# Kernel tuning notes

Hardware: AMD Instinct MI355X
Metric: run time of the kernel (lower is better)

## Reference

```python
import jax, jax.numpy as jnp
import numpy as np

B, S, HID, NH, AH, F = 1024, 100, 128, 2, 64, 2
DH = HID // NH          # item/pos head size = 64
DA = AH // NH           # attribute head size = 32
EPS = 1e-12


def setup_inputs() -> dict:
    key = jax.random.key(0)
    ks = iter(jax.random.split(key, 32))
    n = lambda shape, s=0.02: jax.random.normal(next(ks), shape, dtype=jnp.float32) * s
    inp = {
        "input_tensor": jax.random.normal(next(ks), (B, S, HID), dtype=jnp.float32),
        "attribute_table": jax.random.normal(next(ks), (F, B, S, AH), dtype=jnp.float32),
        "position_embedding": jax.random.normal(next(ks), (B, S, HID), dtype=jnp.float32),
        "attention_mask": jnp.zeros((B, 1, S, S), dtype=jnp.float32),
        # item / positional projections (stored [in, out])
        "Wq": n((HID, HID)), "bq": jnp.zeros((HID,), jnp.float32),
        "Wk": n((HID, HID)), "bk": jnp.zeros((HID,), jnp.float32),
        "Wv": n((HID, HID)), "bv": jnp.zeros((HID,), jnp.float32),
        "Wqp": n((HID, HID)), "bqp": jnp.zeros((HID,), jnp.float32),
        "Wkp": n((HID, HID)), "bkp": jnp.zeros((HID,), jnp.float32),
        # per-attribute projections, stacked over feat axis
        "Wq_attr": n((F, AH, AH)), "bq_attr": jnp.zeros((F, AH), jnp.float32),
        "Wk_attr": n((F, AH, AH)), "bk_attr": jnp.zeros((F, AH), jnp.float32),
        # gate fusion (VanillaAttentionX): Linear(S,S) -> ReLU -> Linear(S,1)
        "fuse_W1": n((S, S)), "fuse_b1": jnp.zeros((S,), jnp.float32),
        "fuse_W2": n((S, 1)), "fuse_b2": jnp.zeros((1,), jnp.float32),
        # output dense + LayerNorm
        "Wd": n((HID, HID)), "bd": jnp.zeros((HID,), jnp.float32),
        "ln_g": jnp.ones((HID,), jnp.float32), "ln_b": jnp.zeros((HID,), jnp.float32),
    }
    return inp


def _split_heads(x, nh):  # [B,S,nh*d] -> [B,nh,S,d]
    b, s, hd = x.shape
    return x.reshape(b, s, nh, hd // nh).transpose(0, 2, 1, 3)


def reference(input_tensor, attribute_table, position_embedding, attention_mask,
              Wq, bq, Wk, bk, Wv, bv, Wqp, bqp, Wkp, bkp,
              Wq_attr, bq_attr, Wk_attr, bk_attr,
              fuse_W1, fuse_b1, fuse_W2, fuse_b2,
              Wd, bd, ln_g, ln_b):
    b, s, hid = input_tensor.shape
    # item / positional QKV
    q = _split_heads(input_tensor @ Wq + bq, NH)
    k = _split_heads(input_tensor @ Wk + bk, NH)
    v = _split_heads(input_tensor @ Wv + bv, NH)
    qp = _split_heads(position_embedding @ Wqp + bqp, NH)
    kp = _split_heads(position_embedding @ Wkp + bkp, NH)
    item_scores = jnp.einsum('bhqd,bhkd->bhqk', q, k)
    pos_scores = jnp.einsum('bhqd,bhkd->bhqk', qp, kp)
    # attribute score streams: [F,B,S,AH] -> [F,B,NH,S,DA]
    aq = jnp.einsum('fbsa,fao->fbso', attribute_table, Wq_attr) + bq_attr[:, None, None, :]
    ak = jnp.einsum('fbsa,fao->fbso', attribute_table, Wk_attr) + bk_attr[:, None, None, :]
    aq = aq.reshape(F, b, s, NH, DA).transpose(0, 1, 3, 2, 4)
    ak = ak.reshape(F, b, s, NH, DA).transpose(0, 1, 3, 2, 4)
    attr_scores = jnp.einsum('fbhqd,fbhkd->fbhqk', aq, ak)  # [F,B,NH,S,S]
    # gate fusion: stack streams on axis -2 -> [B,NH,S,F+2,S]
    stacked = jnp.concatenate([
        jnp.moveaxis(attr_scores, 0, 3),
        item_scores[:, :, :, None, :],
        pos_scores[:, :, :, None, :],
    ], axis=-2)
    energy = jax.nn.relu(stacked @ fuse_W1 + fuse_b1) @ fuse_W2 + fuse_b2  # [B,NH,S,F+2,1]
    gate_w = jax.nn.softmax(energy[..., 0], axis=-1)                       # [B,NH,S,F+2]
    fused = jnp.einsum('bhsfk,bhsf->bhsk', stacked, gate_w)                # [B,NH,S,S]
    scores = fused / jnp.sqrt(jnp.asarray(DH, fused.dtype)) + attention_mask
    probs = jax.nn.softmax(scores, axis=-1)
    ctx = jnp.einsum('bhqk,bhkd->bhqd', probs, v)
    ctx = ctx.transpose(0, 2, 1, 3).reshape(b, s, hid)
    h = ctx @ Wd + bd + input_tensor
    mu = jnp.mean(h, axis=-1, keepdims=True)
    var = jnp.mean((h - mu) ** 2, axis=-1, keepdims=True)
    return (h - mu) / jnp.sqrt(var + EPS) * ln_g + ln_b
```

## Files before the change

kernel.cpp:

```cpp
#include <hip/hip_runtime.h>
#include <hip/hip_bf16.h>

using bf16 = __hip_bfloat16;
using u16 = unsigned short;
typedef __attribute__((ext_vector_type(8))) short bf16x8;
typedef __attribute__((ext_vector_type(16))) float f32x16;

namespace {

constexpr int B_  = 1024;
constexpr int Sd  = 100;
constexpr int BS_ = B_ * Sd;

constexpr int NTHR = 1024;
constexpr int NW   = 16;

constexpr int STP = 420;
constexpr int STS = 104;
constexpr int QKP = 196;
constexpr int AP  = 132;
constexpr int ATP = 68;
constexpr int W1P = 116;
constexpr int VTP = 116;

constexpr int O_ST = 0;
constexpr int O_Q  = 84000;
constexpr int O_K  = 123200;
constexpr int E2S  = 32000;
constexpr int LBYTES = 162400;

constexpr int WQT_E  = 0;
constexpr int WKT_E  = 16384;
constexpr int WQPT_E = 32768;
constexpr int WKPT_E = 49152;
constexpr int WVT_E  = 65536;
constexpr int WAT_E  = 81920;
constexpr int W1T_E  = 98304;
constexpr int WDT_E  = 113152;
constexpr size_t WS_NEED = 129536ull * 2;

__device__ __forceinline__ float bfr(u16 u) {
  unsigned int x = ((unsigned int)u) << 16;
  float f; __builtin_memcpy(&f, &x, 4); return f;
}
__device__ __forceinline__ u16 f2bu(float x) {
  bf16 h = __float2bfloat16(x);
  u16 u; __builtin_memcpy(&u, &h, 2); return u;
}
__device__ __forceinline__ float4 ld4(const float* p) {
  return *reinterpret_cast<const float4*>(p);
}
__device__ __forceinline__ float wsum(float v) {
#pragma unroll
  for (int m = 32; m > 0; m >>= 1) v += __shfl_xor(v, m);
  return v;
}
__device__ __forceinline__ float wmax(float v) {
#pragma unroll
  for (int m = 32; m > 0; m >>= 1) v = fmaxf(v, __shfl_xor(v, m));
  return v;
}

__device__ __forceinline__ f32x16 zf16() {
  f32x16 z;
#pragma unroll
  for (int i = 0; i < 16; ++i) z[i] = 0.f;
  return z;
}
__device__ __forceinline__ f32x16 MFMA32(bf16x8 a, bf16x8 b, f32x16 c) {
  return __builtin_amdgcn_mfma_f32_32x32x16_bf16(a, b, c, 0, 0, 0);
}

__device__ __forceinline__ bf16x8 ld8(const u16* p) {
  const ushort4 a = *reinterpret_cast<const ushort4*>(p);
  const ushort4 b = *reinterpret_cast<const ushort4*>(p + 4);
  bf16x8 f;
  f[0] = (short)a.x; f[1] = (short)a.y; f[2] = (short)a.z; f[3] = (short)a.w;
  f[4] = (short)b.x; f[5] = (short)b.y; f[6] = (short)b.z; f[7] = (short)b.w;
  return f;
}

template <int L4>
__device__ __forceinline__ void stage_rows4(const float* __restrict__ src, u16* dst,
                                            int nrow, int pitch, int tid, int nthr) {
  for (int i = tid; i < (nrow << L4); i += nthr) {
    const int rr = i >> L4, cc = (i & ((1 << L4) - 1)) << 2;
    const float4 v = *reinterpret_cast<const float4*>(src + ((size_t)rr << (L4 + 2)) + cc);
    ushort4 o;
    o.x = f2bu(v.x); o.y = f2bu(v.y); o.z = f2bu(v.z); o.w = f2bu(v.w);
    *reinterpret_cast<ushort4*>(dst + rr * pitch + cc) = o;
  }
}
template <int LC>
__device__ __forceinline__ void stage_wt(const float* __restrict__ W, int ldw, int coff,
                                         u16* dst, int kd, int pitch, int tid, int nthr) {
  constexpr int NC = 1 << LC;
  for (int idx = tid; idx < NC * kd; idx += nthr) {
    const int k = idx >> LC, c = idx & (NC - 1);
    dst[c * pitch + k] = f2bu(W[k * ldw + coff + c]);
  }
}
__device__ __forceinline__ void copy_w64(const u16* __restrict__ src, u16* dst,
                                         int tid, int nthr) {
  for (int i = tid; i < 2048; i += nthr) {
    const int r = i >> 5, c4 = (i & 31) << 2;
    *reinterpret_cast<ushort4*>(dst + r * AP + c4) =
        *reinterpret_cast<const ushort4*>(src + r * 128 + c4);
  }
}

template <int KD, bool TR>
__device__ __forceinline__ void tile32(const u16* A, int apitch, const u16* Wt, int wpitch,
                                       const float* __restrict__ bias, u16* dst, int dpitch,
                                       int dbase, int m0, int n0, int l) {
  const int cr = l & 31, g = l >> 5;
  int ar = m0 + cr; if (ar >= Sd) ar = Sd - 1;
  const u16* ap = A + ar * apitch + g * 8;
  const u16* bp = Wt + (n0 + cr) * wpitch + g * 8;
  f32x16 acc = zf16();
#pragma unroll
  for (int k0 = 0; k0 < KD; k0 += 16)
    acc = MFMA32(ld8(ap + k0), ld8(bp + k0), acc);
  const float bvv = bias[n0 + cr];
#pragma unroll
  for (int i = 0; i < 16; ++i) {
    const int row = m0 + (i & 3) + 8 * (i >> 2) + 4 * g;
    if (row < Sd) {
      if (TR) dst[(n0 + cr) * dpitch + dbase + row] = f2bu(acc[i] + bvv);
      else    dst[row * dpitch + dbase + n0 + cr]   = f2bu(acc[i] + bvv);
    }
  }
}

__global__ __launch_bounds__(256) void prep_weights(
    const float* __restrict__ Wq, const float* __restrict__ Wk,
    const float* __restrict__ Wqp, const float* __restrict__ Wkp,
    const float* __restrict__ Wv, const float* __restrict__ Wqa,
    const float* __restrict__ Wka, const float* __restrict__ W1,
    const float* __restrict__ Wd, u16* __restrict__ ws) {
  const int t = blockIdx.x * 256 + threadIdx.x;
  const int NT = gridDim.x * 256;
  const float* srcs[5] = {Wq, Wk, Wqp, Wkp, Wv};
#pragma unroll
  for (int wsel = 0; wsel < 5; ++wsel) {
    u16* dst = ws + wsel * 16384;
    const float* src = srcs[wsel];
    for (int i = t; i < 16384; i += NT) {
      const int h = i >> 13, c = (i >> 7) & 63, k = i & 127;
      dst[i] = f2bu(src[k * 128 + h * 64 + c]);
    }
  }
  for (int i = t; i < 16384; i += NT) {
    const int pr = i >> 12, h = (i >> 11) & 1, c = (i >> 6) & 31, k = i & 63;
    const float* src = (pr & 1) ? Wka : Wqa;
    ws[WAT_E + i] = f2bu(src[(pr >> 1) * 4096 + k * 64 + h * 32 + c]);
  }
  for (int i = t; i < 14848; i += NT) {
    const int c = i / W1P, k = i - c * W1P;
    ws[W1T_E + i] = (c < Sd && k < Sd) ? f2bu(W1[k * Sd + c]) : (u16)0;
  }
  for (int i = t; i < 16384; i += NT) {
    const int c = i >> 7, k = i & 127;
    ws[WDT_E + i] = f2bu(Wd[k * 128 + c]);
  }
}

template <bool PREP>
__global__ __launch_bounds__(NTHR) void attn_mega(
    const float* __restrict__ input, const float* __restrict__ attrT,
    const float* __restrict__ posE, const float* __restrict__ mask,
    const float* __restrict__ Wq, const float* __restrict__ bq,
    const float* __restrict__ Wk, const float* __restrict__ bk,
    const float* __restrict__ Wv, const float* __restrict__ bv,
    const float* __restrict__ Wqp, const float* __restrict__ bqp,
    const float* __restrict__ Wkp, const float* __restrict__ bkp,
    const float* __restrict__ Wqa, const float* __restrict__ bqa,
    const float* __restrict__ Wka, const float* __restrict__ bka,
    const float* __restrict__ W1, const float* __restrict__ b1,
    const float* __restrict__ W2, const u16* __restrict__ wsw,
    float* __restrict__ ctx) {
  __shared__ __align__(16) char L[LBYTES];
  u16* const ST = (u16*)(L + O_ST);
  u16* const QC = (u16*)(L + O_Q);
  u16* const KC = (u16*)(L + O_K);
  u16* const SA  = (u16*)(L + O_ST);
  u16* const SW1 = (u16*)(L + O_ST + 26400);
  u16* const SW2 = (u16*)(L + O_ST + 43296);
  u16* const AT0  = (u16*)(L + O_ST);
  u16* const AT1  = (u16*)(L + O_ST + 13600);
  u16* const WA0Q = (u16*)(L + O_ST + 27200);
  u16* const WA0K = (u16*)(L + O_ST + 31552);
  u16* const WA1Q = (u16*)(L + O_ST + 35904);
  u16* const WA1K = (u16*)(L + O_ST + 40256);
  u16* const W1T = (u16*)(L + O_K);
  float* const e2s = (float*)(L + O_K + E2S);
  u16* const VA  = (u16*)(L + O_Q);
  u16* const WVT = (u16*)(L + O_K);
  u16* const VT  = (u16*)(L + O_K + 16896);

  const int tid = threadIdx.x;
  const int bh = blockIdx.x;
  const int b = bh >> 1, h = bh & 1;
  const size_t row0 = (size_t)b * Sd;
  const int l = tid & 63, w = tid >> 6;
  const int cr = l & 31, g = l >> 5;

  stage_rows4<5>(input + row0 * 128, SA, 100, AP, tid, NTHR);
  if constexpr (PREP) {
    copy_w64(wsw + WQT_E + h * 8192, SW1, tid, NTHR);
    copy_w64(wsw + WKT_E + h * 8192, SW2, tid, NTHR);
  } else {
    stage_wt<6>(Wq, 128, h * 64, SW1, 128, AP, tid, NTHR);
    stage_wt<6>(Wk, 128, h * 64, SW2, 128, AP, tid, NTHR);
  }
  float4 r2[8];
#pragma unroll
  for (int s = 0; s < 8; ++s) {
    if (PREP && s >= 4) break;
    const int fi = tid + s * NTHR;
    if (fi < 3200) {
      r2[s] = ld4(posE + row0 * 128 + fi * 4);
    } else if (!PREP && fi < 5248) {
      const int f2 = fi - 3200, k = f2 >> 4, c0 = (f2 & 15) << 2;
      r2[s] = ld4(Wqp + k * 128 + h * 64 + c0);
    } else if (!PREP && fi < 7296) {
      const int f2 = fi - 5248, k = f2 >> 4, c0 = (f2 & 15) << 2;
      r2[s] = ld4(Wkp + k * 128 + h * 64 + c0);
    }
  }
  __syncthreads();

  {
    const int pr = w >> 3, mt = (w >> 1) & 3, nt = w & 1;
    tile32<128, false>(SA, AP, pr ? SW2 : SW1, AP, (pr ? bk : bq) + h * 64,
                       pr ? KC : QC, QKP, 0, mt * 32, nt * 32, l);
  }
  __syncthreads();

#pragma unroll
  for (int s = 0; s < 8; ++s) {
    if (PREP && s >= 4) break;
    const int fi = tid + s * NTHR;
    if (fi < 3200) {
      ushort4 o;
      o.x = f2bu(r2[s].x); o.y = f2bu(r2[s].y); o.z = f2bu(r2[s].z); o.w = f2bu(r2[s].w);
      *reinterpret_cast<ushort4*>(SA + (fi >> 5) * AP + ((fi & 31) << 2)) = o;
    } else if (!PREP && fi < 5248) {
      const int f2 = fi - 3200, k = f2 >> 4, c0 = (f2 & 15) << 2;
      SW1[c0 * AP + k] = f2bu(r2[s].x); SW1[(c0 + 1) * AP + k] = f2bu(r2[s].y);
      SW1[(c0 + 2) * AP + k] = f2bu(r2[s].z); SW1[(c0 + 3) * AP + k] = f2bu(r2[s].w);
    } else if (!PREP && fi < 7296) {
      const int f2 = fi - 5248, k = f2 >> 4, c0 = (f2 & 15) << 2;
      SW2[c0 * AP + k] = f2bu(r2[s].x); SW2[(c0 + 1) * AP + k] = f2bu(r2[s].y);
      SW2[(c0 + 2) * AP + k] = f2bu(r2[s].z); SW2[(c0 + 3) * AP + k] = f2bu(r2[s].w);
    }
  }
  if constexpr (PREP) {
    copy_w64(wsw + WQPT_E + h * 8192, SW1, tid, NTHR);
    copy_w64(wsw + WKPT_E + h * 8192, SW2, tid, NTHR);
  }
  float4 r3[6];
#pragma unroll
  for (int s = 0; s < 6; ++s) {
    if (PREP && s >= 4) break;
    const int fi = tid + s * NTHR;
    if (fi < 1600) {
      r3[s] = ld4(attrT + (size_t)b * 6400 + fi * 4);
    } else if (fi < 3200) {
      r3[s] = ld4(attrT + (size_t)(B_ + b) * 6400 + (fi - 1600) * 4);
    } else if (!PREP && fi < 5248) {
      const int f3 = fi - 3200, which = f3 >> 9, fj = f3 & 511;
      const int k = fj >> 3, c0 = (fj & 7) << 2;
      const float* src = (which == 0) ? Wqa : (which == 1) ? Wka
                       : (which == 2) ? (Wqa + 4096) : (Wka + 4096);
      r3[s] = ld4(src + k * 64 + h * 32 + c0);
    }
  }
  __syncthreads();

  {
    const int pr = w >> 3, mt = (w >> 1) & 3, nt = w & 1;
    tile32<128, false>(SA, AP, pr ? SW2 : SW1, AP, (pr ? bkp : bqp) + h * 64,
                       pr ? KC : QC, QKP, 64, mt * 32, nt * 32, l);
  }
  __syncthreads();

#pragma unroll
  for (int s = 0; s < 6; ++s) {
    if (PREP && s >= 4) break;
    const int fi = tid + s * NTHR;
    if (fi < 1600) {
      ushort4 o;
      o.x = f2bu(r3[s].x); o.y = f2bu(r3[s].y); o.z = f2bu(r3[s].z); o.w = f2bu(r3[s].w);
      *reinterpret_cast<ushort4*>(AT0 + (fi >> 4) * ATP + ((fi & 15) << 2)) = o;
    } else if (fi < 3200) {
      const int f3 = fi - 1600;
      ushort4 o;
      o.x = f2bu(r3[s].x); o.y = f2bu(r3[s].y); o.z = f2bu(r3[s].z); o.w = f2bu(r3[s].w);
      *reinterpret_cast<ushort4*>(AT1 + (f3 >> 4) * ATP + ((f3 & 15) << 2)) = o;
    } else if (!PREP && fi < 5248) {
      const int f3 = fi - 3200, which = f3 >> 9, fj = f3 & 511;
      const int k = fj >> 3, c0 = (fj & 7) << 2;
      u16* dst = (which == 0) ? WA0Q : (which == 1) ? WA0K
               : (which == 2) ? WA1Q : WA1K;
      dst[c0 * ATP + k] = f2bu(r3[s].x); dst[(c0 + 1) * ATP + k] = f2bu(r3[s].y);
      dst[(c0 + 2) * ATP + k] = f2bu(r3[s].z); dst[(c0 + 3) * ATP + k] = f2bu(r3[s].w);
    }
  }
  if constexpr (PREP) {
    for (int i = tid; i < 2048; i += NTHR) {
      const int pr = i >> 9, row = (i >> 4) & 31, c4 = (i & 15) << 2;
      u16* dst = (pr == 0) ? WA0Q : (pr == 1) ? WA0K : (pr == 2) ? WA1Q : WA1K;
      *reinterpret_cast<ushort4*>(dst + row * ATP + c4) =
          *reinterpret_cast<const ushort4*>(wsw + WAT_E + pr * 4096 + h * 2048 + row * 64 + c4);
    }
  }
  float4 r5[3];
  ushort4 rw1[4];
  if constexpr (PREP) {
#pragma unroll
    for (int s = 0; s < 4; ++s) {
      const int fi = tid + s * NTHR;
      if (fi < 3712) rw1[s] = reinterpret_cast<const ushort4*>(wsw + W1T_E)[fi];
    }
  } else {
#pragma unroll
    for (int s = 0; s < 3; ++s) {
      const int fi = tid + s * NTHR;
      if (fi < 2500) r5[s] = ld4(W1 + fi * 4);
    }
  }
  __syncthreads();

  {
    const int pr = w >> 2, mt = w & 3;
    const u16* Asrc = (pr < 2) ? AT0 : AT1;
    const u16* Wt = (pr == 0) ? WA0Q : (pr == 1) ? WA0K : (pr == 2) ? WA1Q : WA1K;
    const float* bs = (pr == 0) ? bqa + h * 32 : (pr == 1) ? bka + h * 32
                     : (pr == 2) ? bqa + 64 + h * 32 : bka + 64 + h * 32;
    tile32<64, false>(Asrc, ATP, Wt, ATP, bs, (pr & 1) ? KC : QC, QKP,
                      128 + (pr >> 1) * 32, mt * 32, 0, l);
  }
  __syncthreads();

  {
    ushort4 z; z.x = z.y = z.z = z.w = 0;
    for (int q = tid; q < Sd; q += NTHR)
      *reinterpret_cast<ushort4*>(ST + q * STP + 416) = z;
  }
  {
    const int mt = w >> 2, nt = w & 3;
    const int m0 = mt * 32, n0 = nt * 32;
    int ar = m0 + cr; if (ar >= Sd) ar = Sd - 1;
    int br = n0 + cr; if (br >= Sd) br = Sd - 1;
    const u16* ap = QC + ar * QKP + g * 8;
    const u16* bp = KC + br * QKP + g * 8;
    f32x16 ai = zf16(), po = zf16(), a0 = zf16(), a1 = zf16();
    ai = MFMA32(ld8(ap + 0),   ld8(bp + 0),   ai);
    ai = MFMA32(ld8(ap + 16),  ld8(bp + 16),  ai);
    ai = MFMA32(ld8(ap + 32),  ld8(bp + 32),  ai);
    ai = MFMA32(ld8(ap + 48),  ld8(bp + 48),  ai);
    po = MFMA32(ld8(ap + 64),  ld8(bp + 64),  po);
    po = MFMA32(ld8(ap + 80),  ld8(bp + 80),  po);
    po = MFMA32(ld8(ap + 96),  ld8(bp + 96),  po);
    po = MFMA32(ld8(ap + 112), ld8(bp + 112), po);
    a0 = MFMA32(ld8(ap + 128), ld8(bp + 128), a0);
    a0 = MFMA32(ld8(ap + 144), ld8(bp + 144), a0);
    a1 = MFMA32(ld8(ap + 160), ld8(bp + 160), a1);
    a1 = MFMA32(ld8(ap + 176), ld8(bp + 176), a1);
    const int col = n0 + cr;
    if (col < STS) {
#pragma unroll
      for (int i = 0; i < 16; ++i) {
        const int row = m0 + (i & 3) + 8 * (i >> 2) + 4 * g;
        if (row < Sd) {
          u16* sp = ST + row * STP + col;
          sp[0]       = f2bu(a0[i]);
          sp[STS]     = f2bu(a1[i]);
          sp[2 * STS] = f2bu(ai[i]);
          sp[3 * STS] = f2bu(po[i]);
        }
      }
    }
  }
  __syncthreads();

  if constexpr (PREP) {
#pragma unroll
    for (int s = 0; s < 4; ++s) {
      const int fi = tid + s * NTHR;
      if (fi < 3712) reinterpret_cast<ushort4*>(W1T)[fi] = rw1[s];
    }
  } else {
    {
      ushort4 z; z.x = z.y = z.z = z.w = 0;
      if (tid < 812)
        *reinterpret_cast<ushort4*>(W1T + 11600 + tid * 4) = z;
      if (tid < 400) {
        const int c = tid >> 2, kq = 100 + ((tid & 3) << 2);
        *reinterpret_cast<ushort4*>(W1T + c * W1P + kq) = z;
      }
    }
#pragma unroll
    for (int s = 0; s < 3; ++s) {
      const int fi = tid + s * NTHR;
      if (fi < 2500) {
#pragma unroll
        for (int j = 0; j < 4; ++j) {
          const int o = fi * 4 + j;
          const int k = o / 100, c = o - k * 100;
          W1T[c * W1P + k] = f2bu((j == 0) ? r5[s].x : (j == 1) ? r5[s].y
                                  : (j == 2) ? r5[s].z : r5[s].w);
        }
      }
    }
  }
  __syncthreads();

  {
    float b1v[4], w2v[4];
#pragma unroll
    for (int nt = 0; nt < 4; ++nt) {
      const int c = nt * 32 + cr;
      b1v[nt] = (c < Sd) ? b1[c] : 0.f;
      w2v[nt] = (c < Sd) ? W2[c] : 0.f;
    }
    for (int mt = w; mt < 13; mt += NW) {
      const int m0 = mt * 32;
      int gr = m0 + cr; if (gr > 399) gr = 399;
      const u16* ap = ST + (gr >> 2) * STP + (gr & 3) * STS + g * 8;
      f32x16 c0 = zf16(), c1 = zf16(), c2 = zf16(), c3 = zf16();
#pragma unroll
      for (int k0 = 0; k0 < 112; k0 += 16) {
        const bf16x8 af = ld8(ap + k0);
        c0 = MFMA32(af, ld8(W1T + (cr)      * W1P + g * 8 + k0), c0);
        c1 = MFMA32(af, ld8(W1T + (32 + cr) * W1P + g * 8 + k0), c1);
        c2 = MFMA32(af, ld8(W1T + (64 + cr) * W1P + g * 8 + k0), c2);
        c3 = MFMA32(af, ld8(W1T + (96 + cr) * W1P + g * 8 + k0), c3);
      }
#pragma unroll
      for (int i = 0; i < 16; ++i) {
        float v = fmaxf(c0[i] + b1v[0], 0.f) * w2v[0]
                + fmaxf(c1[i] + b1v[1], 0.f) * w2v[1]
                + fmaxf(c2[i] + b1v[2], 0.f) * w2v[2]
                + fmaxf(c3[i] + b1v[3], 0.f) * w2v[3];
#pragma unroll
        for (int mm = 1; mm < 32; mm <<= 1) v += __shfl_xor(v, mm);
        if (cr == 0) {
          const int go = m0 + (i & 3) + 8 * (i >> 2) + 4 * g;
          if (go < 400) e2s[go] = v;
        }
      }
    }
  }
  __syncthreads();

  stage_rows4<5>(input + row0 * 128, VA, 100, AP, tid, NTHR);
  if constexpr (PREP) {
    copy_w64(wsw + WVT_E + h * 8192, WVT, tid, NTHR);
  } else {
    stage_wt<6>(Wv, 128, h * 64, WVT, 128, AP, tid, NTHR);
  }
  {
    ushort4 z; z.x = z.y = z.z = z.w = 0;
    for (int i2 = tid; i2 < 64 * VTP / 4; i2 += NTHR)
      *reinterpret_cast<ushort4*>(VT + i2 * 4) = z;
  }
  for (int q = w; q < Sd; q += NW) {
    const float* ez = e2s + q * 4;
    float e0 = ez[0], e1 = ez[1], e2v = ez[2], e3 = ez[3];
    const float mg = fmaxf(fmaxf(e0, e1), fmaxf(e2v, e3));
    e0 = __expf(e0 - mg); e1 = __expf(e1 - mg);
    e2v = __expf(e2v - mg); e3 = __expf(e3 - mg);
    const float ginv = 1.0f / (e0 + e1 + e2v + e3);
    const float g0v = e0 * ginv, g1v = e1 * ginv, g2v = e2v * ginv, g3v = e3 * ginv;
    u16* const sp = ST + q * STP;
    const float* const mp = mask + (size_t)b * 10000 + q * 100;
    float x1 = g0v * bfr(sp[l]) + g1v * bfr(sp[STS + l]) +
               g2v * bfr(sp[2 * STS + l]) + g3v * bfr(sp[3 * STS + l]);
    x1 = x1 * 0.125f + mp[l];
    const bool v2 = (l < 36);
    float x2 = -3e38f;
    if (v2) {
      const int k2 = 64 + l;
      x2 = g0v * bfr(sp[k2]) + g1v * bfr(sp[STS + k2]) +
           g2v * bfr(sp[2 * STS + k2]) + g3v * bfr(sp[3 * STS + k2]);
      x2 = x2 * 0.125f + mp[k2];
    }
    const float M = wmax(fmaxf(x1, x2));
    const float ea = __expf(x1 - M);
    const float eb = v2 ? __expf(x2 - M) : 0.f;
    const float inv = 1.0f / wsum(ea + eb);
    sp[l] = f2bu(ea * inv);
    if (v2) sp[64 + l] = f2bu(eb * inv);
  }
  __syncthreads();

  if (w < 8) {
    const int mt = w >> 1, nt = w & 1;
    tile32<128, true>(VA, AP, WVT, AP, bv + h * 64, VT, VTP, 0, mt * 32, nt * 32, l);
  }
  __syncthreads();

  if (w < 8) {
    const int mt = w >> 1, nt = w & 1;
    const int m0 = mt * 32, n0 = nt * 32;
    int ar = m0 + cr; if (ar >= Sd) ar = Sd - 1;
    const u16* ap = ST + ar * STP + g * 8;
    const u16* bp = VT + (n0 + cr) * VTP + g * 8;
    f32x16 acc = zf16();
#pragma unroll
    for (int k0 = 0; k0 < 112; k0 += 16)
      acc = MFMA32(ld8(ap + k0), ld8(bp + k0), acc);
#pragma unroll
    for (int i = 0; i < 16; ++i) {
      const int row = m0 + (i & 3) + 8 * (i >> 2) + 4 * g;
      if (row < Sd)
        ctx[(row0 + row) * 128 + h * 64 + n0 + cr] = acc[i];
    }
  }
}

template <bool PREP>
__global__ __launch_bounds__(512) void dense_ln(
    const float* __restrict__ ctxg, const float* __restrict__ Wd,
    const float* __restrict__ bd, const float* __restrict__ resid,
    const float* __restrict__ lng, const float* __restrict__ lnb,
    const u16* __restrict__ wsw, float* __restrict__ out) {
  __shared__ __align__(16) char L[101376];
  u16* const Ab  = (u16*)L;
  u16* const WdT = (u16*)(L + 33792);
  u16* const Hs  = (u16*)(L + 67584);
  const int tid = threadIdx.x;
  const size_t row0 = (size_t)blockIdx.x * 128;
  const int l = tid & 63, w = tid >> 6, cr = l & 31, g = l >> 5;

  stage_rows4<5>(ctxg + row0 * 128, Ab, 128, AP, tid, 512);
  if constexpr (PREP) {
    for (int i = tid; i < 4096; i += 512) {
      const int r = i >> 5, c4 = (i & 31) << 2;
      *reinterpret_cast<ushort4*>(WdT + r * AP + c4) =
          *reinterpret_cast<const ushort4*>(wsw + WDT_E + r * 128 + c4);
    }
  } else {
    stage_wt<7>(Wd, 128, 0, WdT, 128, AP, tid, 512);
  }
  __syncthreads();

  for (int u = w; u < 16; u += 8) {
    const int m0 = (u >> 2) * 32, n0 = (u & 3) * 32;
    const u16* ap = Ab + (m0 + cr) * AP + g * 8;
    const u16* bp = WdT + (n0 + cr) * AP + g * 8;
    f32x16 acc = zf16();
#pragma unroll
    for (int k0 = 0; k0 < 128; k0 += 16)
      acc = MFMA32(ld8(ap + k0), ld8(bp + k0), acc);
#pragma unroll
    for (int i = 0; i < 16; ++i) {
      const int row = m0 + (i & 3) + 8 * (i >> 2) + 4 * g;
      Hs[row * AP + n0 + cr] = f2bu(acc[i]);
    }
  }
  __syncthreads();

  for (int rr = w; rr < 128; rr += 8) {
    const size_t grow = row0 + rr;
    const float h1 = bfr(Hs[rr * AP + l])      + bd[l]      + resid[grow * 128 + l];
    const float h2 = bfr(Hs[rr * AP + 64 + l]) + bd[64 + l] + resid[grow * 128 + 64 + l];
    const float mu = wsum(h1 + h2) * (1.0f / 128.0f);
    const float d1 = h1 - mu, d2 = h2 - mu;
    const float var = wsum(d1 * d1 + d2 * d2) * (1.0f / 128.0f);
    const float rs = rsqrtf(var + 1e-12f);
    out[grow * 128 + l]      = d1 * rs * lng[l]      + lnb[l];
    out[grow * 128 + 64 + l] = d2 * rs * lng[64 + l] + lnb[64 + l];
  }
}

}

extern "C" void kernel_launch(void* const* d_in, const int* in_sizes, int n_in,
                              void* d_out, int out_size, void* d_ws,
                              size_t ws_size, hipStream_t stream) {
  (void)in_sizes; (void)n_in; (void)out_size;

  const float* input = (const float*)d_in[0];
  const float* attrT = (const float*)d_in[1];
  const float* posE  = (const float*)d_in[2];
  const float* mask  = (const float*)d_in[3];
  const float* Wq  = (const float*)d_in[4];  const float* bq  = (const float*)d_in[5];
  const float* Wk  = (const float*)d_in[6];  const float* bk  = (const float*)d_in[7];
  const float* Wv  = (const float*)d_in[8];  const float* bv  = (const float*)d_in[9];
  const float* Wqp = (const float*)d_in[10]; const float* bqp = (const float*)d_in[11];
  const float* Wkp = (const float*)d_in[12]; const float* bkp = (const float*)d_in[13];
  const float* Wqa = (const float*)d_in[14]; const float* bqa = (const float*)d_in[15];
  const float* Wka = (const float*)d_in[16]; const float* bka = (const float*)d_in[17];
  const float* W1  = (const float*)d_in[18]; const float* b1  = (const float*)d_in[19];
  const float* W2  = (const float*)d_in[20];
  const float* Wd  = (const float*)d_in[22]; const float* bd  = (const float*)d_in[23];
  const float* lng = (const float*)d_in[24]; const float* lnb = (const float*)d_in[25];

  float* ctx = (float*)d_out;

  if (ws_size >= WS_NEED) {
    u16* wsw = (u16*)d_ws;
    prep_weights<<<dim3(128), dim3(256), 0, stream>>>(
        Wq, Wk, Wqp, Wkp, Wv, Wqa, Wka, W1, Wd, wsw);
    attn_mega<true><<<dim3(B_ * 2), dim3(NTHR), 0, stream>>>(
        input, attrT, posE, mask, Wq, bq, Wk, bk, Wv, bv, Wqp, bqp, Wkp, bkp,
        Wqa, bqa, Wka, bka, W1, b1, W2, wsw, ctx);
    dense_ln<true><<<dim3(BS_ / 128), dim3(512), 0, stream>>>(
        ctx, Wd, bd, input, lng, lnb, wsw, ctx);
  } else {
    attn_mega<false><<<dim3(B_ * 2), dim3(NTHR), 0, stream>>>(
        input, attrT, posE, mask, Wq, bq, Wk, bk, Wv, bv, Wqp, bqp, Wkp, bkp,
        Wqa, bqa, Wka, bka, W1, b1, W2, nullptr, ctx);
    dense_ln<false><<<dim3(BS_ / 128), dim3(512), 0, stream>>>(
        ctx, Wd, bd, input, lng, lnb, nullptr, ctx);
  }
}
```

Baseline: 326.6 us.

## Read pre-transposed bf16 weights from global memory directly in MFMA tiles

```diff
diff --git a/kernel.cpp b/kernel.cpp
--- a/kernel.cpp
+++ b/kernel.cpp
@@ -20,13 +20,18 @@
 constexpr int QKP = 196;
 constexpr int AP  = 132;
 constexpr int ATP = 68;
+constexpr int VTP = 116;
 constexpr int W1P = 116;
-constexpr int VTP = 116;
-
-constexpr int O_ST = 0;
-constexpr int O_Q  = 84000;
-constexpr int O_K  = 123200;
-constexpr int E2S  = 32000;
+
+constexpr int O_ST  = 0;
+constexpr int O_SA0 = 0;
+constexpr int O_SA1 = 26400;
+constexpr int O_AT0 = 52800;
+constexpr int O_AT1 = 66400;
+constexpr int O_Q   = 84000;
+constexpr int O_K   = 123200;
+constexpr int O_VT  = 123200;
+constexpr int O_E2S = 139200;
 constexpr int LBYTES = 162400;
 
 constexpr int WQT_E  = 0;
@@ -36,8 +41,9 @@
 constexpr int WVT_E  = 65536;
 constexpr int WAT_E  = 81920;
 constexpr int W1T_E  = 98304;
-constexpr int WDT_E  = 113152;
-constexpr size_t WS_NEED = 129536ull * 2;
+constexpr int WDT_E  = 112640;
+constexpr int W1PG   = 112;
+constexpr size_t WS_NEED = 129024ull * 2;
 
 __device__ __forceinline__ float bfr(u16 u) {
   unsigned int x = ((unsigned int)u) << 16;
@@ -60,7 +66,6 @@
   for (int m = 32; m > 0; m >>= 1) v = fmaxf(v, __shfl_xor(v, m));
   return v;
 }
-
 __device__ __forceinline__ f32x16 zf16() {
   f32x16 z;
 #pragma unroll
@@ -78,6 +83,9 @@
   f[0] = (short)a.x; f[1] = (short)a.y; f[2] = (short)a.z; f[3] = (short)a.w;
   f[4] = (short)b.x; f[5] = (short)b.y; f[6] = (short)b.z; f[7] = (short)b.w;
   return f;
+}
+__device__ __forceinline__ bf16x8 ld8a(const u16* p) {
+  return *reinterpret_cast<const bf16x8*>(p);
 }
 
 template <int L4>
@@ -100,16 +108,12 @@
     dst[c * pitch + k] = f2bu(W[k * ldw + coff + c]);
   }
 }
-__device__ __forceinline__ void copy_w64(const u16* __restrict__ src, u16* dst,
-                                         int tid, int nthr) {
-  for (int i = tid; i < 2048; i += nthr) {
-    const int r = i >> 5, c4 = (i & 31) << 2;
-    *reinterpret_cast<ushort4*>(dst + r * AP + c4) =
-        *reinterpret_cast<const ushort4*>(src + r * 128 + c4);
-  }
-}
-
-template <int KD, bool TR>
+__device__ __forceinline__ void stage_wt6(const float* __restrict__ W, int coff,
+                                          u16* dst, int tid, int nthr) {
+  stage_wt<6>(W, 128, coff, dst, 128, AP, tid, nthr);
+}
+
+template <int KD, bool TR, bool GB>
 __device__ __forceinline__ void tile32(const u16* A, int apitch, const u16* Wt, int wpitch,
                                        const float* __restrict__ bias, u16* dst, int dpitch,
                                        int dbase, int m0, int n0, int l) {
@@ -120,7 +124,7 @@
   f32x16 acc = zf16();
 #pragma unroll
   for (int k0 = 0; k0 < KD; k0 += 16)
-    acc = MFMA32(ld8(ap + k0), ld8(bp + k0), acc);
+    acc = MFMA32(ld8(ap + k0), GB ? ld8a(bp + k0) : ld8(bp + k0), acc);
   const float bvv = bias[n0 + cr];
 #pragma unroll
   for (int i = 0; i < 16; ++i) {
@@ -155,8 +159,8 @@
     const float* src = (pr & 1) ? Wka : Wqa;
     ws[WAT_E + i] = f2bu(src[(pr >> 1) * 4096 + k * 64 + h * 32 + c]);
   }
-  for (int i = t; i < 14848; i += NT) {
-    const int c = i / W1P, k = i - c * W1P;
+  for (int i = t; i < 14336; i += NT) {
+    const int c = i / W1PG, k = i - c * W1PG;
     ws[W1T_E + i] = (c < Sd && k < Sd) ? f2bu(W1[k * Sd + c]) : (u16)0;
   }
   for (int i = t; i < 16384; i += NT) {
@@ -165,38 +169,26 @@
   }
 }
 
-template <bool PREP>
-__global__ __launch_bounds__(NTHR) void attn_mega(
+__global__ __launch_bounds__(NTHR) void attn_mega_p(
     const float* __restrict__ input, const float* __restrict__ attrT,
     const float* __restrict__ posE, const float* __restrict__ mask,
-    const float* __restrict__ Wq, const float* __restrict__ bq,
-    const float* __restrict__ Wk, const float* __restrict__ bk,
-    const float* __restrict__ Wv, const float* __restrict__ bv,
-    const float* __restrict__ Wqp, const float* __restrict__ bqp,
-    const float* __restrict__ Wkp, const float* __restrict__ bkp,
-    const float* __restrict__ Wqa, const float* __restrict__ bqa,
-    const float* __restrict__ Wka, const float* __restrict__ bka,
-    const float* __restrict__ W1, const float* __restrict__ b1,
+    const float* __restrict__ bq, const float* __restrict__ bk,
+    const float* __restrict__ bv, const float* __restrict__ bqp,
+    const float* __restrict__ bkp, const float* __restrict__ bqa,
+    const float* __restrict__ bka, const float* __restrict__ b1,
     const float* __restrict__ W2, const u16* __restrict__ wsw,
     float* __restrict__ ctx) {
   __shared__ __align__(16) char L[LBYTES];
-  u16* const ST = (u16*)(L + O_ST);
-  u16* const QC = (u16*)(L + O_Q);
-  u16* const KC = (u16*)(L + O_K);
-  u16* const SA  = (u16*)(L + O_ST);
-  u16* const SW1 = (u16*)(L + O_ST + 26400);
-  u16* const SW2 = (u16*)(L + O_ST + 43296);
-  u16* const AT0  = (u16*)(L + O_ST);
-  u16* const AT1  = (u16*)(L + O_ST + 13600);
-  u16* const WA0Q = (u16*)(L + O_ST + 27200);
-  u16* const WA0K = (u16*)(L + O_ST + 31552);
-  u16* const WA1Q = (u16*)(L + O_ST + 35904);
-  u16* const WA1K = (u16*)(L + O_ST + 40256);
-  u16* const W1T = (u16*)(L + O_K);
-  float* const e2s = (float*)(L + O_K + E2S);
+  u16* const ST  = (u16*)(L + O_ST);
+  u16* const SA0 = (u16*)(L + O_SA0);
+  u16* const SA1 = (u16*)(L + O_SA1);
+  u16* const AT0 = (u16*)(L + O_AT0);
+  u16* const AT1 = (u16*)(L + O_AT1);
+  u16* const QC  = (u16*)(L + O_Q);
+  u16* const KC  = (u16*)(L + O_K);
   u16* const VA  = (u16*)(L + O_Q);
-  u16* const WVT = (u16*)(L + O_K);
-  u16* const VT  = (u16*)(L + O_K + 16896);
+  u16* const VT  = (u16*)(L + O_VT);
+  float* const e2s = (float*)(L + O_E2S);
 
   const int tid = threadIdx.x;
   const int bh = blockIdx.x;
@@ -205,89 +197,41 @@
   const int l = tid & 63, w = tid >> 6;
   const int cr = l & 31, g = l >> 5;
 
-  stage_rows4<5>(input + row0 * 128, SA, 100, AP, tid, NTHR);
-  if constexpr (PREP) {
-    copy_w64(wsw + WQT_E + h * 8192, SW1, tid, NTHR);
-    copy_w64(wsw + WKT_E + h * 8192, SW2, tid, NTHR);
-  } else {
-    stage_wt<6>(Wq, 128, h * 64, SW1, 128, AP, tid, NTHR);
-    stage_wt<6>(Wk, 128, h * 64, SW2, 128, AP, tid, NTHR);
-  }
-  float4 r2[8];
-#pragma unroll
-  for (int s = 0; s < 8; ++s) {
-    if (PREP && s >= 4) break;
-    const int fi = tid + s * NTHR;
-    if (fi < 3200) {
-      r2[s] = ld4(posE + row0 * 128 + fi * 4);
-    } else if (!PREP && fi < 5248) {
-      const int f2 = fi - 3200, k = f2 >> 4, c0 = (f2 & 15) << 2;
-      r2[s] = ld4(Wqp + k * 128 + h * 64 + c0);
-    } else if (!PREP && fi < 7296) {
-      const int f2 = fi - 5248, k = f2 >> 4, c0 = (f2 & 15) << 2;
-      r2[s] = ld4(Wkp + k * 128 + h * 64 + c0);
-    }
-  }
-  __syncthreads();
-
-  {
-    const int pr = w >> 3, mt = (w >> 1) & 3, nt = w & 1;
-    tile32<128, false>(SA, AP, pr ? SW2 : SW1, AP, (pr ? bk : bq) + h * 64,
-                       pr ? KC : QC, QKP, 0, mt * 32, nt * 32, l);
-  }
-  __syncthreads();
-
-#pragma unroll
-  for (int s = 0; s < 8; ++s) {
-    if (PREP && s >= 4) break;
+  stage_rows4<5>(input + row0 * 128, SA0, 100, AP, tid, NTHR);
+  float4 r2[4];
+#pragma unroll
+  for (int s = 0; s < 4; ++s) {
+    const int fi = tid + s * NTHR;
+    if (fi < 3200) r2[s] = ld4(posE + row0 * 128 + fi * 4);
+  }
+  __syncthreads();
+
+  float4 r3[4];
+#pragma unroll
+  for (int s = 0; s < 4; ++s) {
+    const int fi = tid + s * NTHR;
+    if (fi < 1600)      r3[s] = ld4(attrT + (size_t)b * 6400 + fi * 4);
+    else if (fi < 3200) r3[s] = ld4(attrT + (size_t)(B_ + b) * 6400 + (fi - 1600) * 4);
+  }
+#pragma unroll
+  for (int s = 0; s < 4; ++s) {
     const int fi = tid + s * NTHR;
     if (fi < 3200) {
       ushort4 o;
       o.x = f2bu(r2[s].x); o.y = f2bu(r2[s].y); o.z = f2bu(r2[s].z); o.w = f2bu(r2[s].w);
-      *reinterpret_cast<ushort4*>(SA + (fi >> 5) * AP + ((fi & 31) << 2)) = o;
-    } else if (!PREP && fi < 5248) {
-      const int f2 = fi - 3200, k = f2 >> 4, c0 = (f2 & 15) << 2;
-      SW1[c0 * AP + k] = f2bu(r2[s].x); SW1[(c0 + 1) * AP + k] = f2bu(r2[s].y);
-      SW1[(c0 + 2) * AP + k] = f2bu(r2[s].z); SW1[(c0 + 3) * AP + k] = f2bu(r2[s].w);
-    } else if (!PREP && fi < 7296) {
-      const int f2 = fi - 5248, k = f2 >> 4, c0 = (f2 & 15) << 2;
-      SW2[c0 * AP + k] = f2bu(r2[s].x); SW2[(c0 + 1) * AP + k] = f2bu(r2[s].y);
-      SW2[(c0 + 2) * AP + k] = f2bu(r2[s].z); SW2[(c0 + 3) * AP + k] = f2bu(r2[s].w);
-    }
-  }
-  if constexpr (PREP) {
-    copy_w64(wsw + WQPT_E + h * 8192, SW1, tid, NTHR);
-    copy_w64(wsw + WKPT_E + h * 8192, SW2, tid, NTHR);
-  }
-  float4 r3[6];
-#pragma unroll
-  for (int s = 0; s < 6; ++s) {
-    if (PREP && s >= 4) break;
-    const int fi = tid + s * NTHR;
-    if (fi < 1600) {
-      r3[s] = ld4(attrT + (size_t)b * 6400 + fi * 4);
-    } else if (fi < 3200) {
-      r3[s] = ld4(attrT + (size_t)(B_ + b) * 6400 + (fi - 1600) * 4);
-    } else if (!PREP && fi < 5248) {
-      const int f3 = fi - 3200, which = f3 >> 9, fj = f3 & 511;
-      const int k = fj >> 3, c0 = (fj & 7) << 2;
-      const float* src = (which == 0) ? Wqa : (which == 1) ? Wka
-                       : (which == 2) ? (Wqa + 4096) : (Wka + 4096);
-      r3[s] = ld4(src + k * 64 + h * 32 + c0);
-    }
-  }
-  __syncthreads();
-
+      *reinterpret_cast<ushort4*>(SA1 + (fi >> 5) * AP + ((fi & 31) << 2)) = o;
+    }
+  }
   {
     const int pr = w >> 3, mt = (w >> 1) & 3, nt = w & 1;
-    tile32<128, false>(SA, AP, pr ? SW2 : SW1, AP, (pr ? bkp : bqp) + h * 64,
-                       pr ? KC : QC, QKP, 64, mt * 32, nt * 32, l);
-  }
-  __syncthreads();
-
-#pragma unroll
-  for (int s = 0; s < 6; ++s) {
-    if (PREP && s >= 4) break;
+    const u16* wg = wsw + (pr ? WKT_E : WQT_E) + h * 8192;
+    tile32<128, false, true>(SA0, AP, wg, 128, (pr ? bk : bq) + h * 64,
+                             pr ? KC : QC, QKP, 0, mt * 32, nt * 32, l);
+  }
+  __syncthreads();
+
+#pragma unroll
+  for (int s = 0; s < 4; ++s) {
     const int fi = tid + s * NTHR;
     if (fi < 1600) {
       ushort4 o;
@@ -298,48 +242,24 @@
       ushort4 o;
       o.x = f2bu(r3[s].x); o.y = f2bu(r3[s].y); o.z = f2bu(r3[s].z); o.w = f2bu(r3[s].w);
       *reinterpret_cast<ushort4*>(AT1 + (f3 >> 4) * ATP + ((f3 & 15) << 2)) = o;
-    } else if (!PREP && fi < 5248) {
-      const int f3 = fi - 3200, which = f3 >> 9, fj = f3 & 511;
-      const int k = fj >> 3, c0 = (fj & 7) << 2;
-      u16* dst = (which == 0) ? WA0Q : (which == 1) ? WA0K
-               : (which == 2) ? WA1Q : WA1K;
-      dst[c0 * ATP + k] = f2bu(r3[s].x); dst[(c0 + 1) * ATP + k] = f2bu(r3[s].y);
-      dst[(c0 + 2) * ATP + k] = f2bu(r3[s].z); dst[(c0 + 3) * ATP + k] = f2bu(r3[s].w);
-    }
-  }
-  if constexpr (PREP) {
-    for (int i = tid; i < 2048; i += NTHR) {
-      const int pr = i >> 9, row = (i >> 4) & 31, c4 = (i & 15) << 2;
-      u16* dst = (pr == 0) ? WA0Q : (pr == 1) ? WA0K : (pr == 2) ? WA1Q : WA1K;
-      *reinterpret_cast<ushort4*>(dst + row * ATP + c4) =
-          *reinterpret_cast<const ushort4*>(wsw + WAT_E + pr * 4096 + h * 2048 + row * 64 + c4);
-    }
-  }
-  float4 r5[3];
-  ushort4 rw1[4];
-  if constexpr (PREP) {
-#pragma unroll
-    for (int s = 0; s < 4; ++s) {
-      const int fi = tid + s * NTHR;
-      if (fi < 3712) rw1[s] = reinterpret_cast<const ushort4*>(wsw + W1T_E)[fi];
-    }
-  } else {
-#pragma unroll
-    for (int s = 0; s < 3; ++s) {
-      const int fi = tid + s * NTHR;
-      if (fi < 2500) r5[s] = ld4(W1 + fi * 4);
-    }
+    }
+  }
+  {
+    const int pr = w >> 3, mt = (w >> 1) & 3, nt = w & 1;
+    const u16* wg = wsw + (pr ? WKPT_E : WQPT_E) + h * 8192;
+    tile32<128, false, true>(SA1, AP, wg, 128, (pr ? bkp : bqp) + h * 64,
+                             pr ? KC : QC, QKP, 64, mt * 32, nt * 32, l);
   }
   __syncthreads();
 
   {
     const int pr = w >> 2, mt = w & 3;
     const u16* Asrc = (pr < 2) ? AT0 : AT1;
-    const u16* Wt = (pr == 0) ? WA0Q : (pr == 1) ? WA0K : (pr == 2) ? WA1Q : WA1K;
+    const u16* wg = wsw + WAT_E + pr * 4096 + h * 2048;
     const float* bs = (pr == 0) ? bqa + h * 32 : (pr == 1) ? bka + h * 32
                      : (pr == 2) ? bqa + 64 + h * 32 : bka + 64 + h * 32;
-    tile32<64, false>(Asrc, ATP, Wt, ATP, bs, (pr & 1) ? KC : QC, QKP,
-                      128 + (pr >> 1) * 32, mt * 32, 0, l);
+    tile32<64, false, true>(Asrc, ATP, wg, 64, bs, (pr & 1) ? KC : QC, QKP,
+                            128 + (pr >> 1) * 32, mt * 32, 0, l);
   }
   __syncthreads();
 
@@ -385,38 +305,355 @@
   }
   __syncthreads();
 
-  if constexpr (PREP) {
-#pragma unroll
-    for (int s = 0; s < 4; ++s) {
-      const int fi = tid + s * NTHR;
-      if (fi < 3712) reinterpret_cast<ushort4*>(W1T)[fi] = rw1[s];
-    }
-  } else {
-    {
-      ushort4 z; z.x = z.y = z.z = z.w = 0;
-      if (tid < 812)
-        *reinterpret_cast<ushort4*>(W1T + 11600 + tid * 4) = z;
-      if (tid < 400) {
-        const int c = tid >> 2, kq = 100 + ((tid & 3) << 2);
-        *reinterpret_cast<ushort4*>(W1T + c * W1P + kq) = z;
+  stage_rows4<5>(input + row0 * 128, VA, 100, AP, tid, NTHR);
+  {
+    ushort4 z; z.x = z.y = z.z = z.w = 0;
+    for (int i2 = tid; i2 < 64 * VTP / 4; i2 += NTHR)
+      *reinterpret_cast<ushort4*>(VT + i2 * 4) = z;
+  }
+  __syncthreads();
+
+  {
+    float b1v[4], w2v[4];
+#pragma unroll
+    for (int nt = 0; nt < 4; ++nt) {
+      const int c = nt * 32 + cr;
+      b1v[nt] = (c < Sd) ? b1[c] : 0.f;
+      w2v[nt] = (c < Sd) ? W2[c] : 0.f;
+    }
+    const u16* wg1 = wsw + W1T_E;
+    for (int mt = w; mt < 13; mt += NW) {
+      const int m0 = mt * 32;
+      int gr = m0 + cr; if (gr > 399) gr = 399;
+      const u16* ap = ST + (gr >> 2) * STP + (gr & 3) * STS + g * 8;
+      f32x16 c0 = zf16(), c1 = zf16(), c2 = zf16(), c3 = zf16();
+#pragma unroll
+      for (int k0 = 0; k0 < 112; k0 += 16) {
+        const bf16x8 af = ld8(ap + k0);
+        c0 = MFMA32(af, ld8a(wg1 + (cr)      * W1PG + g * 8 + k0), c0);
+        c1 = MFMA32(af, ld8a(wg1 + (32 + cr) * W1PG + g * 8 + k0), c1);
+        c2 = MFMA32(af, ld8a(wg1 + (64 + cr) * W1PG + g * 8 + k0), c2);
+        c3 = MFMA32(af, ld8a(wg1 + (96 + cr) * W1PG + g * 8 + k0), c3);
       }
-    }
-#pragma unroll
-    for (int s = 0; s < 3; ++s) {
-      const int fi = tid + s * NTHR;
-      if (fi < 2500) {
-#pragma unroll
-        for (int j = 0; j < 4; ++j) {
-          const int o = fi * 4 + j;
-          const int k = o / 100, c = o - k * 100;
-          W1T[c * W1P + k] = f2bu((j == 0) ? r5[s].x : (j == 1) ? r5[s].y
-                                  : (j == 2) ? r5[s].z : r5[s].w);
+#pragma unroll
+      for (int i = 0; i < 16; ++i) {
+        float v = fmaxf(c0[i] + b1v[0], 0.f) * w2v[0]
+                + fmaxf(c1[i] + b1v[1], 0.f) * w2v[1]
+                + fmaxf(c2[i] + b1v[2], 0.f) * w2v[2]
+                + fmaxf(c3[i] + b1v[3], 0.f) * w2v[3];
+#pragma unroll
+        for (int mm = 1; mm < 32; mm <<= 1) v += __shfl_xor(v, mm);
+        if (cr == 0) {
+          const int go = m0 + (i & 3) + 8 * (i >> 2) + 4 * g;
+          if (go < 400) e2s[go] = v;
         }
       }
     }
   }
   __syncthreads();
 
+  if (w < 8) {
+    for (int q = w; q < Sd; q += 8) {
+      const float* ez = e2s + q * 4;
+      float e0 = ez[0], e1 = ez[1], e2v = ez[2], e3 = ez[3];
+      const float mg = fmaxf(fmaxf(e0, e1), fmaxf(e2v, e3));
+      e0 = __expf(e0 - mg); e1 = __expf(e1 - mg);
+      e2v = __expf(e2v - mg); e3 = __expf(e3 - mg);
+      const float ginv = 1.0f / (e0 + e1 + e2v + e3);
+      const float g0v = e0 * ginv, g1v = e1 * ginv, g2v = e2v * ginv, g3v = e3 * ginv;
+      u16* const sp = ST + q * STP;
+      const float* const mp = mask + (size_t)b * 10000 + q * 100;
+      float x1 = g0v * bfr(sp[l]) + g1v * bfr(sp[STS + l]) +
+                 g2v * bfr(sp[2 * STS + l]) + g3v * bfr(sp[3 * STS + l]);
+      x1 = x1 * 0.125f + mp[l];
+      const bool v2 = (l < 36);
+      float x2 = -3e38f;
+      if (v2) {
+        const int k2 = 64 + l;
+        x2 = g0v * bfr(sp[k2]) + g1v * bfr(sp[STS + k2]) +
+             g2v * bfr(sp[2 * STS + k2]) + g3v * bfr(sp[3 * STS + k2]);
+        x2 = x2 * 0.125f + mp[k2];
+      }
+      const float M = wmax(fmaxf(x1, x2));
+      const float ea = __expf(x1 - M);
+      const float eb = v2 ? __expf(x2 - M) : 0.f;
+      const float inv = 1.0f / wsum(ea + eb);
+      sp[l] = f2bu(ea * inv);
+      if (v2) sp[64 + l] = f2bu(eb * inv);
+    }
+  } else {
+    const int u = w - 8;
+    const int mt = u >> 1, nt = u & 1;
+    tile32<128, true, true>(VA, AP, wsw + WVT_E + h * 8192, 128, bv + h * 64,
+                            VT, VTP, 0, mt * 32, nt * 32, l);
+  }
+  __syncthreads();
+
+  if (w < 8) {
+    const int mt = w >> 1, nt = w & 1;
+    const int m0 = mt * 32, n0 = nt * 32;
+    int ar = m0 + cr; if (ar >= Sd) ar = Sd - 1;
+    const u16* ap = ST + ar * STP + g * 8;
+    const u16* bp = VT + (n0 + cr) * VTP + g * 8;
+    f32x16 acc = zf16();
+#pragma unroll
+    for (int k0 = 0; k0 < 112; k0 += 16)
+      acc = MFMA32(ld8(ap + k0), ld8(bp + k0), acc);
+#pragma unroll
+    for (int i = 0; i < 16; ++i) {
+      const int row = m0 + (i & 3) + 8 * (i >> 2) + 4 * g;
+      if (row < Sd)
+        ctx[(row0 + row) * 128 + h * 64 + n0 + cr] = acc[i];
+    }
+  }
+}
+
+__global__ __launch_bounds__(512, 4) void dense_ln_p(
+    const float* __restrict__ ctxg, const float* __restrict__ bd,
+    const float* __restrict__ resid, const float* __restrict__ lng,
+    const float* __restrict__ lnb, const u16* __restrict__ wsw,
+    float* __restrict__ out) {
+  __shared__ __align__(16) char L[67584];
+  u16* const Ab = (u16*)L;
+  u16* const Hs = (u16*)(L + 33792);
+  const int tid = threadIdx.x;
+  const size_t row0 = (size_t)blockIdx.x * 128;
+  const int l = tid & 63, w = tid >> 6, cr = l & 31, g = l >> 5;
+
+  stage_rows4<5>(ctxg + row0 * 128, Ab, 128, AP, tid, 512);
+  __syncthreads();
+
+  for (int u = w; u < 16; u += 8) {
+    const int m0 = (u >> 2) * 32, n0 = (u & 3) * 32;
+    const u16* ap = Ab + (m0 + cr) * AP + g * 8;
+    const u16* bp = wsw + WDT_E + (n0 + cr) * 128 + g * 8;
+    f32x16 acc = zf16();
+#pragma unroll
+    for (int k0 = 0; k0 < 128; k0 += 16)
+      acc = MFMA32(ld8(ap + k0), ld8a(bp + k0), acc);
+#pragma unroll
+    for (int i = 0; i < 16; ++i) {
+      const int row = m0 + (i & 3) + 8 * (i >> 2) + 4 * g;
+      Hs[row * AP + n0 + cr] = f2bu(acc[i]);
+    }
+  }
+  __syncthreads();
+
+  for (int rr = w; rr < 128; rr += 8) {
+    const size_t grow = row0 + rr;
+    const float h1 = bfr(Hs[rr * AP + l])      + bd[l]      + resid[grow * 128 + l];
+    const float h2 = bfr(Hs[rr * AP + 64 + l]) + bd[64 + l] + resid[grow * 128 + 64 + l];
+    const float mu = wsum(h1 + h2) * (1.0f / 128.0f);
+    const float d1 = h1 - mu, d2 = h2 - mu;
+    const float var = wsum(d1 * d1 + d2 * d2) * (1.0f / 128.0f);
+    const float rs = rsqrtf(var + 1e-12f);
+    out[grow * 128 + l]      = d1 * rs * lng[l]      + lnb[l];
+    out[grow * 128 + 64 + l] = d2 * rs * lng[64 + l] + lnb[64 + l];
+  }
+}
+
+__global__ __launch_bounds__(NTHR) void attn_mega_fb(
+    const float* __restrict__ input, const float* __restrict__ attrT,
+    const float* __restrict__ posE, const float* __restrict__ mask,
+    const float* __restrict__ Wq, const float* __restrict__ bq,
+    const float* __restrict__ Wk, const float* __restrict__ bk,
+    const float* __restrict__ Wv, const float* __restrict__ bv,
+    const float* __restrict__ Wqp, const float* __restrict__ bqp,
+    const float* __restrict__ Wkp, const float* __restrict__ bkp,
+    const float* __restrict__ Wqa, const float* __restrict__ bqa,
+    const float* __restrict__ Wka, const float* __restrict__ bka,
+    const float* __restrict__ W1, const float* __restrict__ b1,
+    const float* __restrict__ W2, float* __restrict__ ctx) {
+  __shared__ __align__(16) char L[LBYTES];
+  u16* const ST = (u16*)(L + O_ST);
+  u16* const QC = (u16*)(L + O_Q);
+  u16* const KC = (u16*)(L + O_K);
+  u16* const SA  = (u16*)(L + O_ST);
+  u16* const SW1 = (u16*)(L + O_ST + 26400);
+  u16* const SW2 = (u16*)(L + O_ST + 43296);
+  u16* const AT0  = (u16*)(L + O_ST);
+  u16* const AT1  = (u16*)(L + O_ST + 13600);
+  u16* const WA0Q = (u16*)(L + O_ST + 27200);
+  u16* const WA0K = (u16*)(L + O_ST + 31552);
+  u16* const WA1Q = (u16*)(L + O_ST + 35904);
+  u16* const WA1K = (u16*)(L + O_ST + 40256);
+  u16* const W1T = (u16*)(L + O_K);
+  float* const e2s = (float*)(L + O_K + 32000);
+  u16* const VA  = (u16*)(L + O_Q);
+  u16* const WVT = (u16*)(L + O_K);
+  u16* const VT  = (u16*)(L + O_K + 16896);
+
+  const int tid = threadIdx.x;
+  const int bh = blockIdx.x;
+  const int b = bh >> 1, h = bh & 1;
+  const size_t row0 = (size_t)b * Sd;
+  const int l = tid & 63, w = tid >> 6;
+  const int cr = l & 31, g = l >> 5;
+
+  stage_rows4<5>(input + row0 * 128, SA, 100, AP, tid, NTHR);
+  stage_wt6(Wq, h * 64, SW1, tid, NTHR);
+  stage_wt6(Wk, h * 64, SW2, tid, NTHR);
+  float4 r2[8];
+#pragma unroll
+  for (int s = 0; s < 8; ++s) {
+    const int fi = tid + s * NTHR;
+    if (fi < 3200) r2[s] = ld4(posE + row0 * 128 + fi * 4);
+    else if (fi < 5248) {
+      const int f2 = fi - 3200, k = f2 >> 4, c0 = (f2 & 15) << 2;
+      r2[s] = ld4(Wqp + k * 128 + h * 64 + c0);
+    } else if (fi < 7296) {
+      const int f2 = fi - 5248, k = f2 >> 4, c0 = (f2 & 15) << 2;
+      r2[s] = ld4(Wkp + k * 128 + h * 64 + c0);
+    }
+  }
+  __syncthreads();
+  {
+    const int pr = w >> 3, mt = (w >> 1) & 3, nt = w & 1;
+    tile32<128, false, false>(SA, AP, pr ? SW2 : SW1, AP, (pr ? bk : bq) + h * 64,
+                              pr ? KC : QC, QKP, 0, mt * 32, nt * 32, l);
+  }
+  __syncthreads();
+#pragma unroll
+  for (int s = 0; s < 8; ++s) {
+    const int fi = tid + s * NTHR;
+    if (fi < 3200) {
+      ushort4 o;
+      o.x = f2bu(r2[s].x); o.y = f2bu(r2[s].y); o.z = f2bu(r2[s].z); o.w = f2bu(r2[s].w);
+      *reinterpret_cast<ushort4*>(SA + (fi >> 5) * AP + ((fi & 31) << 2)) = o;
+    } else if (fi < 5248) {
+      const int f2 = fi - 3200, k = f2 >> 4, c0 = (f2 & 15) << 2;
+      SW1[c0 * AP + k] = f2bu(r2[s].x); SW1[(c0 + 1) * AP + k] = f2bu(r2[s].y);
+      SW1[(c0 + 2) * AP + k] = f2bu(r2[s].z); SW1[(c0 + 3) * AP + k] = f2bu(r2[s].w);
+    } else if (fi < 7296) {
+      const int f2 = fi - 5248, k = f2 >> 4, c0 = (f2 & 15) << 2;
+      SW2[c0 * AP + k] = f2bu(r2[s].x); SW2[(c0 + 1) * AP + k] = f2bu(r2[s].y);
+      SW2[(c0 + 2) * AP + k] = f2bu(r2[s].z); SW2[(c0 + 3) * AP + k] = f2bu(r2[s].w);
+    }
+  }
+  float4 r3[6];
+#pragma unroll
+  for (int s = 0; s < 6; ++s) {
+    const int fi = tid + s * NTHR;
+    if (fi < 1600) r3[s] = ld4(attrT + (size_t)b * 6400 + fi * 4);
+    else if (fi < 3200) r3[s] = ld4(attrT + (size_t)(B_ + b) * 6400 + (fi - 1600) * 4);
+    else if (fi < 5248) {
+      const int f3 = fi - 3200, which = f3 >> 9, fj = f3 & 511;
+      const int k = fj >> 3, c0 = (fj & 7) << 2;
+      const float* src = (which == 0) ? Wqa : (which == 1) ? Wka
+                       : (which == 2) ? (Wqa + 4096) : (Wka + 4096);
+      r3[s] = ld4(src + k * 64 + h * 32 + c0);
+    }
+  }
+  __syncthreads();
+  {
+    const int pr = w >> 3, mt = (w >> 1) & 3, nt = w & 1;
+    tile32<128, false, false>(SA, AP, pr ? SW2 : SW1, AP, (pr ? bkp : bqp) + h * 64,
+                              pr ? KC : QC, QKP, 64, mt * 32, nt * 32, l);
+  }
+  __syncthreads();
+#pragma unroll
+  for (int s = 0; s < 6; ++s) {
+    const int fi = tid + s * NTHR;
+    if (fi < 1600) {
+      ushort4 o;
+      o.x = f2bu(r3[s].x); o.y = f2bu(r3[s].y); o.z = f2bu(r3[s].z); o.w = f2bu(r3[s].w);
+      *reinterpret_cast<ushort4*>(AT0 + (fi >> 4) * ATP + ((fi & 15) << 2)) = o;
+    } else if (fi < 3200) {
+      const int f3 = fi - 1600;
+      ushort4 o;
+      o.x = f2bu(r3[s].x); o.y = f2bu(r3[s].y); o.z = f2bu(r3[s].z); o.w = f2bu(r3[s].w);
+      *reinterpret_cast<ushort4*>(AT1 + (f3 >> 4) * ATP + ((f3 & 15) << 2)) = o;
+    } else if (fi < 5248) {
+      const int f3 = fi - 3200, which = f3 >> 9, fj = f3 & 511;
+      const int k = fj >> 3, c0 = (fj & 7) << 2;
+      u16* dst = (which == 0) ? WA0Q : (which == 1) ? WA0K
+               : (which == 2) ? WA1Q : WA1K;
+      dst[c0 * ATP + k] = f2bu(r3[s].x); dst[(c0 + 1) * ATP + k] = f2bu(r3[s].y);
+      dst[(c0 + 2) * ATP + k] = f2bu(r3[s].z); dst[(c0 + 3) * ATP + k] = f2bu(r3[s].w);
+    }
+  }
+  float4 r5[3];
+#pragma unroll
+  for (int s = 0; s < 3; ++s) {
+    const int fi = tid + s * NTHR;
+    if (fi < 2500) r5[s] = ld4(W1 + fi * 4);
+  }
+  __syncthreads();
+  {
+    const int pr = w >> 2, mt = w & 3;
+    const u16* Asrc = (pr < 2) ? AT0 : AT1;
+    const u16* Wt = (pr == 0) ? WA0Q : (pr == 1) ? WA0K : (pr == 2) ? WA1Q : WA1K;
+    const float* bs = (pr == 0) ? bqa + h * 32 : (pr == 1) ? bka + h * 32
+                     : (pr == 2) ? bqa + 64 + h * 32 : bka + 64 + h * 32;
+    tile32<64, false, false>(Asrc, ATP, Wt, ATP, bs, (pr & 1) ? KC : QC, QKP,
+                             128 + (pr >> 1) * 32, mt * 32, 0, l);
+  }
+  __syncthreads();
+  {
+    ushort4 z; z.x = z.y = z.z = z.w = 0;
+    for (int q = tid; q < Sd; q += NTHR)
+      *reinterpret_cast<ushort4*>(ST + q * STP + 416) = z;
+  }
+  {
+    const int mt = w >> 2, nt = w & 3;
+    const int m0 = mt * 32, n0 = nt * 32;
+    int ar = m0 + cr; if (ar >= Sd) ar = Sd - 1;
+    int br = n0 + cr; if (br >= Sd) br = Sd - 1;
+    const u16* ap = QC + ar * QKP + g * 8;
+    const u16* bp = KC + br * QKP + g * 8;
+    f32x16 ai = zf16(), po = zf16(), a0 = zf16(), a1 = zf16();
+    ai = MFMA32(ld8(ap + 0),   ld8(bp + 0),   ai);
+    ai = MFMA32(ld8(ap + 16),  ld8(bp + 16),  ai);
+    ai = MFMA32(ld8(ap + 32),  ld8(bp + 32),  ai);
+    ai = MFMA32(ld8(ap + 48),  ld8(bp + 48),  ai);
+    po = MFMA32(ld8(ap + 64),  ld8(bp + 64),  po);
+    po = MFMA32(ld8(ap + 80),  ld8(bp + 80),  po);
+    po = MFMA32(ld8(ap + 96),  ld8(bp + 96),  po);
+    po = MFMA32(ld8(ap + 112), ld8(bp + 112), po);
+    a0 = MFMA32(ld8(ap + 128), ld8(bp + 128), a0);
+    a0 = MFMA32(ld8(ap + 144), ld8(bp + 144), a0);
+    a1 = MFMA32(ld8(ap + 160), ld8(bp + 160), a1);
+    a1 = MFMA32(ld8(ap + 176), ld8(bp + 176), a1);
+    const int col = n0 + cr;
+    if (col < STS) {
+#pragma unroll
+      for (int i = 0; i < 16; ++i) {
+        const int row = m0 + (i & 3) + 8 * (i >> 2) + 4 * g;
+        if (row < Sd) {
+          u16* sp = ST + row * STP + col;
+          sp[0]       = f2bu(a0[i]);
+          sp[STS]     = f2bu(a1[i]);
+          sp[2 * STS] = f2bu(ai[i]);
+          sp[3 * STS] = f2bu(po[i]);
+        }
+      }
+    }
+  }
+  __syncthreads();
+  {
+    ushort4 z; z.x = z.y = z.z = z.w = 0;
+    if (tid < 812)
+      *reinterpret_cast<ushort4*>(W1T + 11600 + tid * 4) = z;
+    if (tid < 400) {
+      const int c = tid >> 2, kq = 100 + ((tid & 3) << 2);
+      *reinterpret_cast<ushort4*>(W1T + c * W1P + kq) = z;
+    }
+  }
+  if (tid < 8) ((u16*)(L + O_Q))[tid] = 0;
+#pragma unroll
+  for (int s = 0; s < 3; ++s) {
+    const int fi = tid + s * NTHR;
+    if (fi < 2500) {
+#pragma unroll
+      for (int j = 0; j < 4; ++j) {
+        const int o = fi * 4 + j;
+        const int k = o / 100, c = o - k * 100;
+        W1T[c * W1P + k] = f2bu((j == 0) ? r5[s].x : (j == 1) ? r5[s].y
+                                : (j == 2) ? r5[s].z : r5[s].w);
+      }
+    }
+  }
+  __syncthreads();
   {
     float b1v[4], w2v[4];
 #pragma unroll
@@ -454,13 +691,8 @@
     }
   }
   __syncthreads();
-
   stage_rows4<5>(input + row0 * 128, VA, 100, AP, tid, NTHR);
-  if constexpr (PREP) {
-    copy_w64(wsw + WVT_E + h * 8192, WVT, tid, NTHR);
-  } else {
-    stage_wt<6>(Wv, 128, h * 64, WVT, 128, AP, tid, NTHR);
-  }
+  stage_wt6(Wv, h * 64, WVT, tid, NTHR);
   {
     ushort4 z; z.x = z.y = z.z = z.w = 0;
     for (int i2 = tid; i2 < 64 * VTP / 4; i2 += NTHR)
@@ -495,13 +727,11 @@
     if (v2) sp[64 + l] = f2bu(eb * inv);
   }
   __syncthreads();
-
   if (w < 8) {
     const int mt = w >> 1, nt = w & 1;
-    tile32<128, true>(VA, AP, WVT, AP, bv + h * 64, VT, VTP, 0, mt * 32, nt * 32, l);
-  }
-  __syncthreads();
-
+    tile32<128, true, false>(VA, AP, WVT, AP, bv + h * 64, VT, VTP, 0, mt * 32, nt * 32, l);
+  }
+  __syncthreads();
   if (w < 8) {
     const int mt = w >> 1, nt = w & 1;
     const int m0 = mt * 32, n0 = nt * 32;
@@ -521,12 +751,11 @@
   }
 }
 
-template <bool PREP>
-__global__ __launch_bounds__(512) void dense_ln(
+__global__ __launch_bounds__(512) void dense_ln_fb(
     const float* __restrict__ ctxg, const float* __restrict__ Wd,
     const float* __restrict__ bd, const float* __restrict__ resid,
     const float* __restrict__ lng, const float* __restrict__ lnb,
-    const u16* __restrict__ wsw, float* __restrict__ out) {
+    float* __restrict__ out) {
   __shared__ __align__(16) char L[101376];
   u16* const Ab  = (u16*)L;
   u16* const WdT = (u16*)(L + 33792);
@@ -536,17 +765,8 @@
   const int l = tid & 63, w = tid >> 6, cr = l & 31, g = l >> 5;
 
   stage_rows4<5>(ctxg + row0 * 128, Ab, 128, AP, tid, 512);
-  if constexpr (PREP) {
-    for (int i = tid; i < 4096; i += 512) {
-      const int r = i >> 5, c4 = (i & 31) << 2;
-      *reinterpret_cast<ushort4*>(WdT + r * AP + c4) =
-          *reinterpret_cast<const ushort4*>(wsw + WDT_E + r * 128 + c4);
-    }
-  } else {
-    stage_wt<7>(Wd, 128, 0, WdT, 128, AP, tid, 512);
-  }
-  __syncthreads();
-
+  stage_wt<7>(Wd, 128, 0, WdT, 128, AP, tid, 512);
+  __syncthreads();
   for (int u = w; u < 16; u += 8) {
     const int m0 = (u >> 2) * 32, n0 = (u & 3) * 32;
     const u16* ap = Ab + (m0 + cr) * AP + g * 8;
@@ -562,7 +782,6 @@
     }
   }
   __syncthreads();
-
   for (int rr = w; rr < 128; rr += 8) {
     const size_t grow = row0 + rr;
     const float h1 = bfr(Hs[rr * AP + l])      + bd[l]      + resid[grow * 128 + l];
@@ -605,16 +824,15 @@
     u16* wsw = (u16*)d_ws;
     prep_weights<<<dim3(128), dim3(256), 0, stream>>>(
         Wq, Wk, Wqp, Wkp, Wv, Wqa, Wka, W1, Wd, wsw);
-    attn_mega<true><<<dim3(B_ * 2), dim3(NTHR), 0, stream>>>(
+    attn_mega_p<<<dim3(B_ * 2), dim3(NTHR), 0, stream>>>(
+        input, attrT, posE, mask, bq, bk, bv, bqp, bkp, bqa, bka, b1, W2, wsw, ctx);
+    dense_ln_p<<<dim3(BS_ / 128), dim3(512), 0, stream>>>(
+        ctx, bd, input, lng, lnb, wsw, ctx);
+  } else {
+    attn_mega_fb<<<dim3(B_ * 2), dim3(NTHR), 0, stream>>>(
         input, attrT, posE, mask, Wq, bq, Wk, bk, Wv, bv, Wqp, bqp, Wkp, bkp,
-        Wqa, bqa, Wka, bka, W1, b1, W2, wsw, ctx);
-    dense_ln<true><<<dim3(BS_ / 128), dim3(512), 0, stream>>>(
-        ctx, Wd, bd, input, lng, lnb, wsw, ctx);
-  } else {
-    attn_mega<false><<<dim3(B_ * 2), dim3(NTHR), 0, stream>>>(
-        input, attrT, posE, mask, Wq, bq, Wk, bk, Wv, bv, Wqp, bqp, Wkp, bkp,
-        Wqa, bqa, Wka, bka, W1, b1, W2, nullptr, ctx);
-    dense_ln<false><<<dim3(BS_ / 128), dim3(512), 0, stream>>>(
-        ctx, Wd, bd, input, lng, lnb, nullptr, ctx);
-  }
-}
+        Wqa, bqa, Wka, bka, W1, b1, W2, ctx);
+    dense_ln_fb<<<dim3(BS_ / 128), dim3(512), 0, stream>>>(
+        ctx, Wd, bd, input, lng, lnb, ctx);
+  }
+}
```

New measurement: 397.1 us. 21.6% more time.
